# Optimization experiments

Hardware: AMD Instinct MI355X
Metric: run time of the kernel (lower is better)

## Reference

```python
import jax, jax.numpy as jnp
import numpy as np

D_MODEL, N_HEADS, D_LLM = 1024, 16, 4096
D_KEYS = D_MODEL // N_HEADS  # 64


def setup_inputs() -> dict:
    key = jax.random.key(0)
    ks = jax.random.split(key, 11)
    s = lambda fan_in: 1.0 / np.sqrt(fan_in)
    inp = {
        "target_embedding": jax.random.normal(ks[0], (4, 2048, D_MODEL), jnp.float32),
        "source_embedding": jax.random.normal(ks[1], (4, 1024, D_LLM), jnp.float32),
        "value_embedding": jax.random.normal(ks[2], (4, 1024, D_LLM), jnp.float32),
        "Wq": jax.random.uniform(ks[3], (D_MODEL, D_KEYS * N_HEADS), jnp.float32, -s(D_MODEL), s(D_MODEL)),
        "bq": jax.random.uniform(ks[4], (D_KEYS * N_HEADS,), jnp.float32, -s(D_MODEL), s(D_MODEL)),
        "Wk": jax.random.uniform(ks[5], (D_LLM, D_KEYS * N_HEADS), jnp.float32, -s(D_LLM), s(D_LLM)),
        "bk": jax.random.uniform(ks[6], (D_KEYS * N_HEADS,), jnp.float32, -s(D_LLM), s(D_LLM)),
        "Wv": jax.random.uniform(ks[7], (D_LLM, D_KEYS * N_HEADS), jnp.float32, -s(D_LLM), s(D_LLM)),
        "bv": jax.random.uniform(ks[8], (D_KEYS * N_HEADS,), jnp.float32, -s(D_LLM), s(D_LLM)),
        "Wo": jax.random.uniform(ks[9], (D_KEYS * N_HEADS, D_MODEL), jnp.float32, -s(D_KEYS * N_HEADS), s(D_KEYS * N_HEADS)),
        "bo": jax.random.uniform(ks[10], (D_MODEL,), jnp.float32, -s(D_KEYS * N_HEADS), s(D_KEYS * N_HEADS)),
    }
    return inp


def reference(target_embedding, source_embedding, value_embedding,
              Wq, bq, Wk, bk, Wv, bv, Wo, bo):
    B, L, _ = target_embedding.shape
    _, S, _ = source_embedding.shape
    H, E = N_HEADS, D_KEYS
    q = (target_embedding @ Wq + bq).reshape(B, L, H, E)
    k = (source_embedding @ Wk + bk).reshape(B, S, H, E)
    v = (value_embedding @ Wv + bv).reshape(B, S, H, E)
    scale = 1.0 / np.sqrt(E)
    scores = jnp.einsum('blhe,bshe->bhls', q, k)  # [B,H,L,S]
    A = jax.nn.softmax(scale * scores, axis=-1)   # dropout = identity (eval mode)
    out = jnp.einsum('bhls,bshe->blhe', A, v).reshape(B, L, H * E)
    return out @ Wo + bo
```

## Files before the change

kernel.cpp:

```cpp
#include <hip/hip_runtime.h>
#include <hip/hip_bf16.h>

using bf16 = __hip_bfloat16;
typedef __attribute__((ext_vector_type(8))) short short8;
typedef __attribute__((ext_vector_type(4))) float f32x4;

static constexpr int Bc = 4, Lc = 2048, Sc = 1024;
static constexpr int DModel = 1024;

__device__ __forceinline__ void gload16(const void* g, void* l) {
  __builtin_amdgcn_global_load_lds((const __attribute__((address_space(1))) void*)g,
                                   (__attribute__((address_space(3))) void*)l,
                                   16, 0, 0);
}

__global__ void cvt3(const float* __restrict__ a, bf16* __restrict__ ao, long na4,
                     const float* __restrict__ b, bf16* __restrict__ bo, long nb4,
                     const float* __restrict__ c, bf16* __restrict__ co, long nc4) {
  long total = na4 + nb4 + nc4;
  long stride = (long)gridDim.x * blockDim.x;
  for (long i = (long)blockIdx.x * blockDim.x + threadIdx.x; i < total; i += stride) {
    const float* src; bf16* dst; long j;
    if (i < na4)            { src = a; dst = ao; j = i; }
    else if (i < na4 + nb4) { src = b; dst = bo; j = i - na4; }
    else                    { src = c; dst = co; j = i - na4 - nb4; }
    float4 v = reinterpret_cast<const float4*>(src)[j];
    alignas(8) bf16 t[4] = {__float2bfloat16(v.x), __float2bfloat16(v.y),
                            __float2bfloat16(v.z), __float2bfloat16(v.w)};
    reinterpret_cast<ushort4*>(dst)[j] = *reinterpret_cast<const ushort4*>(t);
  }
}

__global__ __launch_bounds__(256) void transpose_cvt_w(const float* __restrict__ Wq, bf16* __restrict__ WqT,
                                                       const float* __restrict__ Wk, bf16* __restrict__ WkT,
                                                       const float* __restrict__ Wv, bf16* __restrict__ WvT,
                                                       const float* __restrict__ Wo, bf16* __restrict__ WoT) {
  __shared__ bf16 tile[32][33];
  int bid = blockIdx.x;
  const float* in; bf16* out; int R, l;
  if (bid < 1024)      { in = Wq; out = WqT; R = 1024; l = bid; }
  else if (bid < 5120) { in = Wk; out = WkT; R = 4096; l = bid - 1024; }
  else if (bid < 9216) { in = Wv; out = WvT; R = 4096; l = bid - 5120; }
  else                 { in = Wo; out = WoT; R = 1024; l = bid - 9216; }
  const int C = 1024;
  int bx = l & 31, by = l >> 5;
  int tx = threadIdx.x & 31, ty = threadIdx.x >> 5;
  int r0 = by * 32, c0 = bx * 32;
#pragma unroll
  for (int i = 0; i < 32; i += 8)
    tile[ty + i][tx] = __float2bfloat16(in[(long)(r0 + ty + i) * C + c0 + tx]);
  __syncthreads();
#pragma unroll
  for (int i = 0; i < 32; i += 8)
    out[(long)(c0 + ty + i) * R + r0 + tx] = tile[tx][ty + i];
}

__global__ __launch_bounds__(256) void transpose_bf16_batched(const bf16* __restrict__ in,
                                                              bf16* __restrict__ out,
                                                              int R, int C) {
  __shared__ bf16 tile[32][33];
  long base = (long)blockIdx.z * R * C;
  int tx = threadIdx.x & 31, ty = threadIdx.x >> 5;
  int r0 = blockIdx.y * 32, c0 = blockIdx.x * 32;
#pragma unroll
  for (int i = 0; i < 32; i += 8)
    tile[ty + i][tx] = in[base + (long)(r0 + ty + i) * C + c0 + tx];
  __syncthreads();
#pragma unroll
  for (int i = 0; i < 32; i += 8)
    out[base + (long)(c0 + ty + i) * R + r0 + tx] = tile[tx][ty + i];
}

__device__ __forceinline__ void gemm_core(const bf16* __restrict__ A, const bf16* __restrict__ Bt,
                                          const float* __restrict__ bias,
                                          bf16* __restrict__ Cb, float* __restrict__ Cf,
                                          int N, int K, int bx, int by,
                                          bf16* As, bf16* Bs) {
  const int tid = threadIdx.x;
  const int lane = tid & 63, g = lane >> 4, lm = lane & 15;
  const int wid = tid >> 6, wr = wid >> 1, wc = wid & 1;
  const long brow = (long)by * 128, bcol = (long)bx * 128;
  const bf16* Ab = A + brow * K;
  const bf16* Bb = Bt + bcol * K;

  f32x4 zero = {0.f, 0.f, 0.f, 0.f};
  f32x4 acc[4][4];
#pragma unroll
  for (int i = 0; i < 4; ++i)
#pragma unroll
    for (int j = 0; j < 4; ++j) acc[i][j] = zero;

  const char* Asc = (const char*)As;
  const char* Bsc = (const char*)Bs;

  for (int k0 = 0; k0 < K; k0 += 64) {
    __syncthreads();
#pragma unroll
    for (int t = 0; t < 4; ++t) {
      int sl = tid + t * 256;
      int row = sl >> 3;
      int kg = (sl & 7) ^ (row & 7);
      gload16(Ab + (long)row * K + k0 + kg * 8, (char*)As + sl * 16);
      gload16(Bb + (long)row * K + k0 + kg * 8, (char*)Bs + sl * 16);
    }
    __syncthreads();
#pragma unroll
    for (int ks = 0; ks < 2; ++ks) {
      short8 af[4], bfv[4];
#pragma unroll
      for (int mi = 0; mi < 4; ++mi) {
        int m = wr * 64 + mi * 16 + lm;
        af[mi] = *reinterpret_cast<const short8*>(
            Asc + ((m * 128 + ks * 64 + g * 16) ^ ((m & 7) << 4)));
      }
#pragma unroll
      for (int ni = 0; ni < 4; ++ni) {
        int n = wc * 64 + ni * 16 + lm;
        bfv[ni] = *reinterpret_cast<const short8*>(
            Bsc + ((n * 128 + ks * 64 + g * 16) ^ ((n & 7) << 4)));
      }
#pragma unroll
      for (int mi = 0; mi < 4; ++mi)
#pragma unroll
        for (int ni = 0; ni < 4; ++ni)
          acc[mi][ni] = __builtin_amdgcn_mfma_f32_16x16x32_bf16(af[mi], bfv[ni], acc[mi][ni], 0, 0, 0);
    }
  }

#pragma unroll
  for (int ni = 0; ni < 4; ++ni) {
    long n = bcol + wc * 64 + ni * 16 + lm;
    float bv = bias ? bias[n] : 0.f;
#pragma unroll
    for (int mi = 0; mi < 4; ++mi) {
      long m0 = brow + wr * 64 + mi * 16 + g * 4;
#pragma unroll
      for (int r = 0; r < 4; ++r) {
        float o = acc[mi][ni][r] + bv;
        if (Cb) Cb[(m0 + r) * N + n] = __float2bfloat16(o);
        else    Cf[(m0 + r) * N + n] = o;
      }
    }
  }
}

__global__ __launch_bounds__(256) void gemm_bt(const bf16* __restrict__ A,
                                               const bf16* __restrict__ Bt,
                                               const float* __restrict__ bias,
                                               bf16* __restrict__ Cb,
                                               float* __restrict__ Cf,
                                               int N, int K) {
  __shared__ bf16 As[128 * 64];
  __shared__ bf16 Bs[128 * 64];
  gemm_core(A, Bt, bias, Cb, Cf, N, K, blockIdx.x, blockIdx.y, As, Bs);
}

__global__ __launch_bounds__(256) void gemm_qkv(
    const bf16* __restrict__ A0, const bf16* __restrict__ B0, const float* __restrict__ c0, bf16* __restrict__ C0, int K0, int nb0,
    const bf16* __restrict__ A1, const bf16* __restrict__ B1, const float* __restrict__ c1, bf16* __restrict__ C1, int K1, int nb1,
    const bf16* __restrict__ A2, const bf16* __restrict__ B2, const float* __restrict__ c2, bf16* __restrict__ C2, int K2) {
  __shared__ bf16 As[128 * 64];
  __shared__ bf16 Bs[128 * 64];
  int bid = blockIdx.x;
  const bf16 *A, *Bt; const float* bias; bf16* C; int K, l;
  if (bid < nb0)            { A = A0; Bt = B0; bias = c0; C = C0; K = K0; l = bid; }
  else if (bid < nb0 + nb1) { A = A1; Bt = B1; bias = c1; C = C1; K = K1; l = bid - nb0; }
  else                      { A = A2; Bt = B2; bias = c2; C = C2; K = K2; l = bid - nb0 - nb1; }
  gemm_core(A, Bt, bias, C, nullptr, 1024, K, l & 7, l >> 3, As, Bs);
}

__global__ __launch_bounds__(256) void attn_fused(const bf16* __restrict__ q,
                                                  const bf16* __restrict__ k,
                                                  const bf16* __restrict__ vT,
                                                  bf16* __restrict__ o) {
  constexpr float C2 = 0.18033688011112042f;
  constexpr float THR = 6.0f;
  __shared__ bf16 Kl[64 * 64];
  __shared__ bf16 Vl[64 * 64];
  __shared__ bf16 Pl[4][16 * 64];
  const int tid = threadIdx.x;
  const int lane = tid & 63, g = lane >> 4, lm = lane & 15;
  const int wid = tid >> 6;
  const int b = blockIdx.y >> 4, h = blockIdx.y & 15;
  const int qbase = blockIdx.x * 64 + wid * 16;

  const bf16* qrow = q + (long)(b * Lc + qbase + lm) * DModel + h * 64;
  short8 qa0 = *reinterpret_cast<const short8*>(qrow + g * 8);
  short8 qa1 = *reinterpret_cast<const short8*>(qrow + 32 + g * 8);
#pragma unroll
  for (int j = 0; j < 8; ++j) {
    union { ushort u; bf16 h; } cv;
    cv.u = (ushort)qa0[j];
    bf16 s0 = __float2bfloat16(__bfloat162float(cv.h) * C2);
    qa0[j] = (short)*reinterpret_cast<ushort*>(&s0);
    cv.u = (ushort)qa1[j];
    bf16 s1 = __float2bfloat16(__bfloat162float(cv.h) * C2);
    qa1[j] = (short)*reinterpret_cast<ushort*>(&s1);
  }

  const bf16* kbase = k + (long)b * Sc * DModel + h * 64;
  const bf16* vbase = vT + ((long)b * DModel + h * 64) * Sc;

  f32x4 zero = {0.f, 0.f, 0.f, 0.f};
  f32x4 accO[4];
#pragma unroll
  for (int i = 0; i < 4; ++i) accO[i] = zero;
  f32x4 accL = zero;
  float mst[4] = {-1e30f, -1e30f, -1e30f, -1e30f};

  short8 vones;
#pragma unroll
  for (int j = 0; j < 8; ++j) vones[j] = (short)0x3F80;

  const char* Klc = (const char*)Kl;
  const char* Vlc = (const char*)Vl;
  char* Plc = (char*)Pl + wid * (16 * 64 * 2);

  for (int sc0 = 0; sc0 < Sc; sc0 += 64) {
    __syncthreads();
#pragma unroll
    for (int t = 0; t < 2; ++t) {
      int sl = tid + t * 256;
      int row = sl >> 3;
      int cg = (sl & 7) ^ (row & 7);
      gload16(kbase + (long)(sc0 + row) * DModel + cg * 8, (char*)Kl + sl * 16);
      gload16(vbase + (long)row * Sc + sc0 + cg * 8, (char*)Vl + sl * 16);
    }
    __syncthreads();

    f32x4 scv[4];
    __builtin_amdgcn_s_setprio(1);
#pragma unroll
    for (int st = 0; st < 4; ++st) {
      int s = st * 16 + lm;
      int sw = (s & 7) << 4;
      short8 kb0 = *reinterpret_cast<const short8*>(Klc + ((s * 128 + g * 16) ^ sw));
      short8 kb1 = *reinterpret_cast<const short8*>(Klc + ((s * 128 + 64 + g * 16) ^ sw));
      f32x4 z = zero;
      z = __builtin_amdgcn_mfma_f32_16x16x32_bf16(qa0, kb0, z, 0, 0, 0);
      z = __builtin_amdgcn_mfma_f32_16x16x32_bf16(qa1, kb1, z, 0, 0, 0);
      scv[st] = z;
    }
    __builtin_amdgcn_s_setprio(0);

    float pmax[4];
#pragma unroll
    for (int r = 0; r < 4; ++r)
      pmax[r] = fmaxf(fmaxf(scv[0][r], scv[1][r]), fmaxf(scv[2][r], scv[3][r]));
    int need = 0;
#pragma unroll
    for (int r = 0; r < 4; ++r) need |= (pmax[r] > mst[r] + THR) ? 1 : 0;
    if (__any(need)) {
#pragma unroll
      for (int r = 0; r < 4; ++r) {
        float mx = pmax[r];
        mx = fmaxf(mx, __shfl_xor(mx, 1));
        mx = fmaxf(mx, __shfl_xor(mx, 2));
        mx = fmaxf(mx, __shfl_xor(mx, 4));
        mx = fmaxf(mx, __shfl_xor(mx, 8));
        float mnew = fmaxf(mst[r], mx);
        float corr = __builtin_amdgcn_exp2f(mst[r] - mnew);
        mst[r] = mnew;
        accL[r] *= corr;
#pragma unroll
        for (int et = 0; et < 4; ++et) accO[et][r] *= corr;
      }
    }
#pragma unroll
    for (int r = 0; r < 4; ++r) {
      int qq = g * 4 + r;
      int swp = (qq & 7) << 4;
#pragma unroll
      for (int st = 0; st < 4; ++st) {
        float p = __builtin_amdgcn_exp2f(scv[st][r] - mst[r]);
        *reinterpret_cast<bf16*>(Plc + ((qq * 128 + (st * 16 + lm) * 2) ^ swp)) =
            __float2bfloat16(p);
      }
    }

    __builtin_amdgcn_s_setprio(1);
#pragma unroll
    for (int sk = 0; sk < 2; ++sk) {
      short8 pa = *reinterpret_cast<const short8*>(
          Plc + ((lm * 128 + sk * 64 + g * 16) ^ ((lm & 7) << 4)));
      accL = __builtin_amdgcn_mfma_f32_16x16x32_bf16(pa, vones, accL, 0, 0, 0);
#pragma unroll
      for (int et = 0; et < 4; ++et) {
        int e = et * 16 + lm;
        short8 vb = *reinterpret_cast<const short8*>(
            Vlc + ((e * 128 + sk * 64 + g * 16) ^ ((e & 7) << 4)));
        accO[et] = __builtin_amdgcn_mfma_f32_16x16x32_bf16(pa, vb, accO[et], 0, 0, 0);
      }
    }
    __builtin_amdgcn_s_setprio(0);
  }

#pragma unroll
  for (int r = 0; r < 4; ++r) {
    float inv = 1.0f / accL[r];
    long row = (long)(b * Lc + qbase + g * 4 + r);
#pragma unroll
    for (int et = 0; et < 4; ++et)
      o[row * DModel + h * 64 + et * 16 + lm] = __float2bfloat16(accO[et][r] * inv);
  }
}

extern "C" void kernel_launch(void* const* d_in, const int* in_sizes, int n_in,
                              void* d_out, int out_size, void* d_ws, size_t ws_size,
                              hipStream_t stream) {
  const float* tgt = (const float*)d_in[0];
  const float* src = (const float*)d_in[1];
  const float* val = (const float*)d_in[2];
  const float* Wq  = (const float*)d_in[3];
  const float* bq  = (const float*)d_in[4];
  const float* Wk  = (const float*)d_in[5];
  const float* bk  = (const float*)d_in[6];
  const float* Wv  = (const float*)d_in[7];
  const float* bv  = (const float*)d_in[8];
  const float* Wo  = (const float*)d_in[9];
  const float* bo  = (const float*)d_in[10];
  float* out = (float*)d_out;
  char* ws = (char*)d_ws;

  const long n4_tgt = (long)8192 * 1024 / 4;
  const long n4_sv  = (long)4096 * 4096 / 4;

  if (ws_size >= (132ul << 20)) {
    bf16* WqT  = (bf16*)(ws + (0l   << 20));
    bf16* WkT  = (bf16*)(ws + (2l   << 20));
    bf16* WvT  = (bf16*)(ws + (10l  << 20));
    bf16* WoT  = (bf16*)(ws + (18l  << 20));
    bf16* tgtb = (bf16*)(ws + (20l  << 20));
    bf16* srcb = (bf16*)(ws + (36l  << 20));
    bf16* valb = (bf16*)(ws + (68l  << 20));
    bf16* qb   = (bf16*)(ws + (100l << 20));
    bf16* kb   = (bf16*)(ws + (116l << 20));
    bf16* vb   = (bf16*)(ws + (124l << 20));
    bf16* vTb   = srcb;
    bf16* attnb = tgtb;

    transpose_cvt_w<<<10240, 256, 0, stream>>>(Wq, WqT, Wk, WkT, Wv, WvT, Wo, WoT);
    cvt3<<<4096, 256, 0, stream>>>(tgt, tgtb, n4_tgt, src, srcb, n4_sv, val, valb, n4_sv);
    gemm_qkv<<<1024, 256, 0, stream>>>(tgtb, WqT, bq, qb, 1024, 512,
                                       srcb, WkT, bk, kb, 4096, 256,
                                       valb, WvT, bv, vb, 4096);
    transpose_bf16_batched<<<dim3(32, 32, 4), 256, 0, stream>>>(vb, vTb, 1024, 1024);
    attn_fused<<<dim3(32, 64), 256, 0, stream>>>(qb, kb, vTb, attnb);
    gemm_bt<<<dim3(8, 64), 256, 0, stream>>>(attnb, WoT, bo, (bf16*)nullptr, out, 1024, 1024);
  } else {
    if (ws_size < (100ul << 20)) return;
    bf16* WqT  = (bf16*)(ws + (0l  << 20));
    bf16* WkT  = (bf16*)(ws + (2l  << 20));
    bf16* WvT  = (bf16*)(ws + (10l << 20));
    bf16* WoT  = (bf16*)(ws + (18l << 20));
    bf16* tgtb = (bf16*)(ws + (20l << 20));
    bf16* srcb = (bf16*)(ws + (36l << 20));
    bf16* qb   = (bf16*)(ws + (68l << 20));
    bf16* kb   = (bf16*)(ws + (84l << 20));
    bf16* vTb  = (bf16*)(ws + (92l << 20));
    bf16* vb = WkT;
    bf16* attnb = tgtb;

    transpose_cvt_w<<<10240, 256, 0, stream>>>(Wq, WqT, Wk, WkT, Wv, WvT, Wo, WoT);
    cvt3<<<4096, 256, 0, stream>>>(tgt, tgtb, n4_tgt, src, srcb, n4_sv,
                                   (const float*)nullptr, (bf16*)nullptr, 0);
    gemm_bt<<<dim3(8, 64), 256, 0, stream>>>(tgtb, WqT, bq, qb, (float*)nullptr, 1024, 1024);
    gemm_bt<<<dim3(8, 32), 256, 0, stream>>>(srcb, WkT, bk, kb, (float*)nullptr, 1024, 4096);
    cvt3<<<4096, 256, 0, stream>>>(val, srcb, n4_sv, (const float*)nullptr, (bf16*)nullptr, 0,
                                   (const float*)nullptr, (bf16*)nullptr, 0);
    gemm_bt<<<dim3(8, 32), 256, 0, stream>>>(srcb, WvT, bv, vb, (float*)nullptr, 1024, 4096);
    transpose_bf16_batched<<<dim3(32, 32, 4), 256, 0, stream>>>(vb, vTb, 1024, 1024);
    attn_fused<<<dim3(32, 64), 256, 0, stream>>>(qb, kb, vTb, attnb);
    gemm_bt<<<dim3(8, 64), 256, 0, stream>>>(attnb, WoT, bo, (bf16*)nullptr, out, 1024, 1024);
  }
}
```

Measured before the change: 274.6 us.

## Double-buffer GEMM and attention LDS tiles; fuse V transpose into QKV epilogue

Adds LDS double-buffering with prefetch of the next K-tile to both the GEMM core and the attention kernel, so each loop iteration needs one barrier and global loads overlap with MFMA work. The V projection now writes its output already transposed from the GEMM epilogue, which removes the separate transpose kernel and its round trip through memory. The QKV launch is reordered so the long-K (K and V) blocks are scheduled first, and the low-workspace fallback path is dropped. In exchange, LDS use per block doubles, which may lower occupancy, and the transposed epilogue issues 8-byte scattered stores.

```diff
diff --git a/kernel.cpp b/kernel.cpp
--- a/kernel.cpp
+++ b/kernel.cpp
@@ -55,33 +55,29 @@
     out[(long)(c0 + ty + i) * R + r0 + tx] = tile[tx][ty + i];
 }
 
-__global__ __launch_bounds__(256) void transpose_bf16_batched(const bf16* __restrict__ in,
-                                                              bf16* __restrict__ out,
-                                                              int R, int C) {
-  __shared__ bf16 tile[32][33];
-  long base = (long)blockIdx.z * R * C;
-  int tx = threadIdx.x & 31, ty = threadIdx.x >> 5;
-  int r0 = blockIdx.y * 32, c0 = blockIdx.x * 32;
-#pragma unroll
-  for (int i = 0; i < 32; i += 8)
-    tile[ty + i][tx] = in[base + (long)(r0 + ty + i) * C + c0 + tx];
-  __syncthreads();
-#pragma unroll
-  for (int i = 0; i < 32; i += 8)
-    out[base + (long)(c0 + ty + i) * R + r0 + tx] = tile[tx][ty + i];
-}
-
 __device__ __forceinline__ void gemm_core(const bf16* __restrict__ A, const bf16* __restrict__ Bt,
                                           const float* __restrict__ bias,
                                           bf16* __restrict__ Cb, float* __restrict__ Cf,
+                                          bf16* __restrict__ Cvt,
                                           int N, int K, int bx, int by,
                                           bf16* As, bf16* Bs) {
   const int tid = threadIdx.x;
   const int lane = tid & 63, g = lane >> 4, lm = lane & 15;
   const int wid = tid >> 6, wr = wid >> 1, wc = wid & 1;
   const long brow = (long)by * 128, bcol = (long)bx * 128;
-  const bf16* Ab = A + brow * K;
-  const bf16* Bb = Bt + bcol * K;
+
+  const bf16* asrc[4];
+  const bf16* bsrc[4];
+  int dsto[4];
+#pragma unroll
+  for (int t = 0; t < 4; ++t) {
+    int sl = tid + t * 256;
+    int row = sl >> 3;
+    int kg = (sl & 7) ^ (row & 7);
+    asrc[t] = A + (brow + row) * (long)K + kg * 8;
+    bsrc[t] = Bt + (bcol + row) * (long)K + kg * 8;
+    dsto[t] = sl * 16;
+  }
 
   f32x4 zero = {0.f, 0.f, 0.f, 0.f};
   f32x4 acc[4][4];
@@ -90,20 +86,32 @@
 #pragma unroll
     for (int j = 0; j < 4; ++j) acc[i][j] = zero;
 
-  const char* Asc = (const char*)As;
-  const char* Bsc = (const char*)Bs;
-
-  for (int k0 = 0; k0 < K; k0 += 64) {
-    __syncthreads();
-#pragma unroll
-    for (int t = 0; t < 4; ++t) {
-      int sl = tid + t * 256;
-      int row = sl >> 3;
-      int kg = (sl & 7) ^ (row & 7);
-      gload16(Ab + (long)row * K + k0 + kg * 8, (char*)As + sl * 16);
-      gload16(Bb + (long)row * K + k0 + kg * 8, (char*)Bs + sl * 16);
-    }
-    __syncthreads();
+  char* Asc = (char*)As;
+  char* Bsc = (char*)Bs;
+
+#pragma unroll
+  for (int t = 0; t < 4; ++t) {
+    gload16(asrc[t], Asc + dsto[t]);
+    gload16(bsrc[t], Bsc + dsto[t]);
+    asrc[t] += 64; bsrc[t] += 64;
+  }
+  __syncthreads();
+
+  const int nt = K >> 6;
+  for (int i = 0; i < nt; ++i) {
+    const int cur = i & 1;
+    if (i + 1 < nt) {
+      const int nxt = cur ^ 1;
+#pragma unroll
+      for (int t = 0; t < 4; ++t) {
+        gload16(asrc[t], Asc + nxt * 16384 + dsto[t]);
+        gload16(bsrc[t], Bsc + nxt * 16384 + dsto[t]);
+        asrc[t] += 64; bsrc[t] += 64;
+      }
+    }
+    const char* Ab = Asc + cur * 16384;
+    const char* Bb = Bsc + cur * 16384;
+    __builtin_amdgcn_s_setprio(1);
 #pragma unroll
     for (int ks = 0; ks < 2; ++ks) {
       short8 af[4], bfv[4];
@@ -111,13 +119,13 @@
       for (int mi = 0; mi < 4; ++mi) {
         int m = wr * 64 + mi * 16 + lm;
         af[mi] = *reinterpret_cast<const short8*>(
-            Asc + ((m * 128 + ks * 64 + g * 16) ^ ((m & 7) << 4)));
+            Ab + ((m * 128 + ks * 64 + g * 16) ^ ((m & 7) << 4)));
       }
 #pragma unroll
       for (int ni = 0; ni < 4; ++ni) {
         int n = wc * 64 + ni * 16 + lm;
         bfv[ni] = *reinterpret_cast<const short8*>(
-            Bsc + ((n * 128 + ks * 64 + g * 16) ^ ((n & 7) << 4)));
+            Bb + ((n * 128 + ks * 64 + g * 16) ^ ((n & 7) << 4)));
       }
 #pragma unroll
       for (int mi = 0; mi < 4; ++mi)
@@ -125,6 +133,8 @@
         for (int ni = 0; ni < 4; ++ni)
           acc[mi][ni] = __builtin_amdgcn_mfma_f32_16x16x32_bf16(af[mi], bfv[ni], acc[mi][ni], 0, 0, 0);
     }
+    __builtin_amdgcn_s_setprio(0);
+    __syncthreads();
   }
 
 #pragma unroll
@@ -134,11 +144,20 @@
 #pragma unroll
     for (int mi = 0; mi < 4; ++mi) {
       long m0 = brow + wr * 64 + mi * 16 + g * 4;
-#pragma unroll
-      for (int r = 0; r < 4; ++r) {
-        float o = acc[mi][ni][r] + bv;
-        if (Cb) Cb[(m0 + r) * N + n] = __float2bfloat16(o);
-        else    Cf[(m0 + r) * N + n] = o;
+      if (Cvt) {
+        long b = m0 >> 10, s0 = m0 & 1023;
+        alignas(8) bf16 t4[4];
+#pragma unroll
+        for (int r = 0; r < 4; ++r) t4[r] = __float2bfloat16(acc[mi][ni][r] + bv);
+        *reinterpret_cast<ushort4*>(Cvt + ((b << 10) + n) * 1024 + s0) =
+            *reinterpret_cast<const ushort4*>(t4);
+      } else {
+#pragma unroll
+        for (int r = 0; r < 4; ++r) {
+          float o = acc[mi][ni][r] + bv;
+          if (Cb) Cb[(m0 + r) * N + n] = __float2bfloat16(o);
+          else    Cf[(m0 + r) * N + n] = o;
+        }
       }
     }
   }
@@ -150,23 +169,23 @@
                                                bf16* __restrict__ Cb,
                                                float* __restrict__ Cf,
                                                int N, int K) {
-  __shared__ bf16 As[128 * 64];
-  __shared__ bf16 Bs[128 * 64];
-  gemm_core(A, Bt, bias, Cb, Cf, N, K, blockIdx.x, blockIdx.y, As, Bs);
+  __shared__ bf16 As[2 * 128 * 64];
+  __shared__ bf16 Bs[2 * 128 * 64];
+  gemm_core(A, Bt, bias, Cb, Cf, nullptr, N, K, blockIdx.x, blockIdx.y, As, Bs);
 }
 
 __global__ __launch_bounds__(256) void gemm_qkv(
-    const bf16* __restrict__ A0, const bf16* __restrict__ B0, const float* __restrict__ c0, bf16* __restrict__ C0, int K0, int nb0,
-    const bf16* __restrict__ A1, const bf16* __restrict__ B1, const float* __restrict__ c1, bf16* __restrict__ C1, int K1, int nb1,
-    const bf16* __restrict__ A2, const bf16* __restrict__ B2, const float* __restrict__ c2, bf16* __restrict__ C2, int K2) {
-  __shared__ bf16 As[128 * 64];
-  __shared__ bf16 Bs[128 * 64];
+    const bf16* __restrict__ Ak, const bf16* __restrict__ Bk, const float* __restrict__ bk_, bf16* __restrict__ Ck, int Kk, int nbk,
+    const bf16* __restrict__ Av, const bf16* __restrict__ Bv_, const float* __restrict__ bv_, bf16* __restrict__ CvT, int Kv, int nbv,
+    const bf16* __restrict__ Aq, const bf16* __restrict__ Bq_, const float* __restrict__ bq_, bf16* __restrict__ Cq, int Kq) {
+  __shared__ bf16 As[2 * 128 * 64];
+  __shared__ bf16 Bs[2 * 128 * 64];
   int bid = blockIdx.x;
-  const bf16 *A, *Bt; const float* bias; bf16* C; int K, l;
-  if (bid < nb0)            { A = A0; Bt = B0; bias = c0; C = C0; K = K0; l = bid; }
-  else if (bid < nb0 + nb1) { A = A1; Bt = B1; bias = c1; C = C1; K = K1; l = bid - nb0; }
-  else                      { A = A2; Bt = B2; bias = c2; C = C2; K = K2; l = bid - nb0 - nb1; }
-  gemm_core(A, Bt, bias, C, nullptr, 1024, K, l & 7, l >> 3, As, Bs);
+  const bf16 *A, *Bt; const float* bias; bf16 *C = nullptr, *Cvt = nullptr; int K, l;
+  if (bid < nbk)            { A = Ak; Bt = Bk;  bias = bk_; C = Ck;    K = Kk; l = bid; }
+  else if (bid < nbk + nbv) { A = Av; Bt = Bv_; bias = bv_; Cvt = CvT; K = Kv; l = bid - nbk; }
+  else                      { A = Aq; Bt = Bq_; bias = bq_; C = Cq;   K = Kq; l = bid - nbk - nbv; }
+  gemm_core(A, Bt, bias, C, nullptr, Cvt, 1024, K, l & 7, l >> 3, As, Bs);
 }
 
 __global__ __launch_bounds__(256) void attn_fused(const bf16* __restrict__ q,
@@ -175,8 +194,8 @@
                                                   bf16* __restrict__ o) {
   constexpr float C2 = 0.18033688011112042f;
   constexpr float THR = 6.0f;
-  __shared__ bf16 Kl[64 * 64];
-  __shared__ bf16 Vl[64 * 64];
+  __shared__ bf16 Kl[2][64 * 64];
+  __shared__ bf16 Vl[2][64 * 64];
   __shared__ bf16 Pl[4][16 * 64];
   const int tid = threadIdx.x;
   const int lane = tid & 63, g = lane >> 4, lm = lane & 15;
@@ -201,6 +220,19 @@
   const bf16* kbase = k + (long)b * Sc * DModel + h * 64;
   const bf16* vbase = vT + ((long)b * DModel + h * 64) * Sc;
 
+  const bf16* ksrc[2];
+  const bf16* vsrc[2];
+  int dsto[2];
+#pragma unroll
+  for (int t = 0; t < 2; ++t) {
+    int sl = tid + t * 256;
+    int row = sl >> 3;
+    int cg = (sl & 7) ^ (row & 7);
+    ksrc[t] = kbase + (long)row * DModel + cg * 8;
+    vsrc[t] = vbase + (long)row * Sc + cg * 8;
+    dsto[t] = sl * 16;
+  }
+
   f32x4 zero = {0.f, 0.f, 0.f, 0.f};
   f32x4 accO[4];
 #pragma unroll
@@ -212,21 +244,31 @@
 #pragma unroll
   for (int j = 0; j < 8; ++j) vones[j] = (short)0x3F80;
 
-  const char* Klc = (const char*)Kl;
-  const char* Vlc = (const char*)Vl;
+  char* Klc = (char*)Kl;
+  char* Vlc = (char*)Vl;
   char* Plc = (char*)Pl + wid * (16 * 64 * 2);
 
-  for (int sc0 = 0; sc0 < Sc; sc0 += 64) {
-    __syncthreads();
-#pragma unroll
-    for (int t = 0; t < 2; ++t) {
-      int sl = tid + t * 256;
-      int row = sl >> 3;
-      int cg = (sl & 7) ^ (row & 7);
-      gload16(kbase + (long)(sc0 + row) * DModel + cg * 8, (char*)Kl + sl * 16);
-      gload16(vbase + (long)row * Sc + sc0 + cg * 8, (char*)Vl + sl * 16);
-    }
-    __syncthreads();
+#pragma unroll
+  for (int t = 0; t < 2; ++t) {
+    gload16(ksrc[t], Klc + dsto[t]);
+    gload16(vsrc[t], Vlc + dsto[t]);
+    ksrc[t] += 64 * DModel; vsrc[t] += 64;
+  }
+  __syncthreads();
+
+  for (int j = 0; j < Sc / 64; ++j) {
+    const int cur = j & 1;
+    if (j + 1 < Sc / 64) {
+      const int nxt = cur ^ 1;
+#pragma unroll
+      for (int t = 0; t < 2; ++t) {
+        gload16(ksrc[t], Klc + nxt * 8192 + dsto[t]);
+        gload16(vsrc[t], Vlc + nxt * 8192 + dsto[t]);
+        ksrc[t] += 64 * DModel; vsrc[t] += 64;
+      }
+    }
+    const char* Kb = Klc + cur * 8192;
+    const char* Vb = Vlc + cur * 8192;
 
     f32x4 scv[4];
     __builtin_amdgcn_s_setprio(1);
@@ -234,8 +276,8 @@
     for (int st = 0; st < 4; ++st) {
       int s = st * 16 + lm;
       int sw = (s & 7) << 4;
-      short8 kb0 = *reinterpret_cast<const short8*>(Klc + ((s * 128 + g * 16) ^ sw));
-      short8 kb1 = *reinterpret_cast<const short8*>(Klc + ((s * 128 + 64 + g * 16) ^ sw));
+      short8 kb0 = *reinterpret_cast<const short8*>(Kb + ((s * 128 + g * 16) ^ sw));
+      short8 kb1 = *reinterpret_cast<const short8*>(Kb + ((s * 128 + 64 + g * 16) ^ sw));
       f32x4 z = zero;
       z = __builtin_amdgcn_mfma_f32_16x16x32_bf16(qa0, kb0, z, 0, 0, 0);
       z = __builtin_amdgcn_mfma_f32_16x16x32_bf16(qa1, kb1, z, 0, 0, 0);
@@ -288,11 +330,12 @@
       for (int et = 0; et < 4; ++et) {
         int e = et * 16 + lm;
         short8 vb = *reinterpret_cast<const short8*>(
-            Vlc + ((e * 128 + sk * 64 + g * 16) ^ ((e & 7) << 4)));
+            Vb + ((e * 128 + sk * 64 + g * 16) ^ ((e & 7) << 4)));
         accO[et] = __builtin_amdgcn_mfma_f32_16x16x32_bf16(pa, vb, accO[et], 0, 0, 0);
       }
     }
     __builtin_amdgcn_s_setprio(0);
+    __syncthreads();
   }
 
 #pragma unroll
@@ -325,52 +368,25 @@
   const long n4_tgt = (long)8192 * 1024 / 4;
   const long n4_sv  = (long)4096 * 4096 / 4;
 
-  if (ws_size >= (132ul << 20)) {
-    bf16* WqT  = (bf16*)(ws + (0l   << 20));
-    bf16* WkT  = (bf16*)(ws + (2l   << 20));
-    bf16* WvT  = (bf16*)(ws + (10l  << 20));
-    bf16* WoT  = (bf16*)(ws + (18l  << 20));
-    bf16* tgtb = (bf16*)(ws + (20l  << 20));
-    bf16* srcb = (bf16*)(ws + (36l  << 20));
-    bf16* valb = (bf16*)(ws + (68l  << 20));
-    bf16* qb   = (bf16*)(ws + (100l << 20));
-    bf16* kb   = (bf16*)(ws + (116l << 20));
-    bf16* vb   = (bf16*)(ws + (124l << 20));
-    bf16* vTb   = srcb;
-    bf16* attnb = tgtb;
-
-    transpose_cvt_w<<<10240, 256, 0, stream>>>(Wq, WqT, Wk, WkT, Wv, WvT, Wo, WoT);
-    cvt3<<<4096, 256, 0, stream>>>(tgt, tgtb, n4_tgt, src, srcb, n4_sv, val, valb, n4_sv);
-    gemm_qkv<<<1024, 256, 0, stream>>>(tgtb, WqT, bq, qb, 1024, 512,
-                                       srcb, WkT, bk, kb, 4096, 256,
-                                       valb, WvT, bv, vb, 4096);
-    transpose_bf16_batched<<<dim3(32, 32, 4), 256, 0, stream>>>(vb, vTb, 1024, 1024);
-    attn_fused<<<dim3(32, 64), 256, 0, stream>>>(qb, kb, vTb, attnb);
-    gemm_bt<<<dim3(8, 64), 256, 0, stream>>>(attnb, WoT, bo, (bf16*)nullptr, out, 1024, 1024);
-  } else {
-    if (ws_size < (100ul << 20)) return;
-    bf16* WqT  = (bf16*)(ws + (0l  << 20));
-    bf16* WkT  = (bf16*)(ws + (2l  << 20));
-    bf16* WvT  = (bf16*)(ws + (10l << 20));
-    bf16* WoT  = (bf16*)(ws + (18l << 20));
-    bf16* tgtb = (bf16*)(ws + (20l << 20));
-    bf16* srcb = (bf16*)(ws + (36l << 20));
-    bf16* qb   = (bf16*)(ws + (68l << 20));
-    bf16* kb   = (bf16*)(ws + (84l << 20));
-    bf16* vTb  = (bf16*)(ws + (92l << 20));
-    bf16* vb = WkT;
-    bf16* attnb = tgtb;
-
-    transpose_cvt_w<<<10240, 256, 0, stream>>>(Wq, WqT, Wk, WkT, Wv, WvT, Wo, WoT);
-    cvt3<<<4096, 256, 0, stream>>>(tgt, tgtb, n4_tgt, src, srcb, n4_sv,
-                                   (const float*)nullptr, (bf16*)nullptr, 0);
-    gemm_bt<<<dim3(8, 64), 256, 0, stream>>>(tgtb, WqT, bq, qb, (float*)nullptr, 1024, 1024);
-    gemm_bt<<<dim3(8, 32), 256, 0, stream>>>(srcb, WkT, bk, kb, (float*)nullptr, 1024, 4096);
-    cvt3<<<4096, 256, 0, stream>>>(val, srcb, n4_sv, (const float*)nullptr, (bf16*)nullptr, 0,
-                                   (const float*)nullptr, (bf16*)nullptr, 0);
-    gemm_bt<<<dim3(8, 32), 256, 0, stream>>>(srcb, WvT, bv, vb, (float*)nullptr, 1024, 4096);
-    transpose_bf16_batched<<<dim3(32, 32, 4), 256, 0, stream>>>(vb, vTb, 1024, 1024);
-    attn_fused<<<dim3(32, 64), 256, 0, stream>>>(qb, kb, vTb, attnb);
-    gemm_bt<<<dim3(8, 64), 256, 0, stream>>>(attnb, WoT, bo, (bf16*)nullptr, out, 1024, 1024);
-  }
-}
+  if (ws_size < (132ul << 20)) return;
+
+  bf16* WqT  = (bf16*)(ws + (0l   << 20));
+  bf16* WkT  = (bf16*)(ws + (2l   << 20));
+  bf16* WvT  = (bf16*)(ws + (10l  << 20));
+  bf16* WoT  = (bf16*)(ws + (18l  << 20));
+  bf16* tgtb = (bf16*)(ws + (20l  << 20));
+  bf16* srcb = (bf16*)(ws + (36l  << 20));
+  bf16* valb = (bf16*)(ws + (68l  << 20));
+  bf16* qb   = (bf16*)(ws + (100l << 20));
+  bf16* kb   = (bf16*)(ws + (116l << 20));
+  bf16* vTb  = (bf16*)(ws + (124l << 20));
+  bf16* attnb = tgtb;
+
+  transpose_cvt_w<<<10240, 256, 0, stream>>>(Wq, WqT, Wk, WkT, Wv, WvT, Wo, WoT);
+  cvt3<<<4096, 256, 0, stream>>>(tgt, tgtb, n4_tgt, src, srcb, n4_sv, val, valb, n4_sv);
+  gemm_qkv<<<1024, 256, 0, stream>>>(srcb, WkT, bk, kb, 4096, 256,
+                                     valb, WvT, bv, vTb, 4096, 256,
+                                     tgtb, WqT, bq, qb, 1024);
+  attn_fused<<<dim3(32, 64), 256, 0, stream>>>(qb, kb, vTb, attnb);
+  gemm_bt<<<dim3(8, 64), 256, 0, stream>>>(attnb, WoT, bo, (bf16*)nullptr, out, 1024, 1024);
+}
```

Result: faster. 268.6 us (-2.2%).
